# Kernel optimization log

Hardware: AMD Instinct MI355X
Metric: run time of the kernel (lower is better)

Reference implementation:

```python
import jax, jax.numpy as jnp
import numpy as np
from jax import lax

B, CIN, H, W = 8, 64, 128, 128
COUT, K = 128, 3
PAD, STRIDE, DIL = 1, 1, 1
KK = K * K


def setup_inputs() -> dict:
    ks = jax.random.split(jax.random.key(0), 6)
    x = jax.random.normal(ks[0], (B, CIN, H, W), jnp.float32)
    pre_w = jax.random.normal(ks[1], (CIN, CIN, 1, 1), jnp.float32) * (1.0 / float(np.sqrt(CIN)))
    pre_b = jnp.zeros((CIN,), jnp.float32)
    off_w = jax.random.normal(ks[2], (2 * KK, CIN, K, K), jnp.float32) * 0.01
    off_b = jnp.zeros((2 * KK,), jnp.float32)
    mod_w = jax.random.normal(ks[3], (KK, CIN, K, K), jnp.float32) * 0.01
    mod_b = jnp.zeros((KK,), jnp.float32)
    reg_w = jax.random.normal(ks[4], (COUT, CIN, K, K), jnp.float32) * (1.0 / float(np.sqrt(CIN * KK)))
    return dict(x=x, pre_w=pre_w, pre_b=pre_b, off_w=off_w, off_b=off_b,
                mod_w=mod_w, mod_b=mod_b, reg_w=reg_w)


def _conv3x3(x, w, b):
    y = lax.conv_general_dilated(x, w, (STRIDE, STRIDE), [(PAD, PAD), (PAD, PAD)],
                                 rhs_dilation=(DIL, DIL),
                                 dimension_numbers=('NCHW', 'OIHW', 'NCHW'))
    return y + b[None, :, None, None]


def _bilinear(img, py, px):
    # img: [C,H,W]; py,px: [KK,Ho,Wo] float coords; zero padding outside image
    Hh, Ww = img.shape[1], img.shape[2]
    y0f = jnp.floor(py)
    x0f = jnp.floor(px)
    wy = py - y0f
    wx = px - x0f
    y0 = y0f.astype(jnp.int32)
    x0 = x0f.astype(jnp.int32)

    def gather(yi, xi):
        valid = (yi >= 0) & (yi < Hh) & (xi >= 0) & (xi < Ww)
        yc = jnp.clip(yi, 0, Hh - 1)
        xc = jnp.clip(xi, 0, Ww - 1)
        return img[:, yc, xc] * valid[None].astype(img.dtype)  # [C,KK,Ho,Wo]

    return (gather(y0, x0) * ((1 - wy) * (1 - wx))[None]
            + gather(y0, x0 + 1) * ((1 - wy) * wx)[None]
            + gather(y0 + 1, x0) * (wy * (1 - wx))[None]
            + gather(y0 + 1, x0 + 1) * (wy * wx)[None])


def _dcn_forward(x, pre_w, pre_b, off_w, off_b, mod_w, mod_b, reg_w):
    # 1x1 channel-mapping conv created in the original forward
    x = lax.conv_general_dilated(x, pre_w, (1, 1), 'VALID',
                                 dimension_numbers=('NCHW', 'OIHW', 'NCHW'))
    x = x + pre_b[None, :, None, None]

    offset = _conv3x3(x, off_w, off_b)                    # [B,2*KK,Ho,Wo]
    mask = 2.0 * jax.nn.sigmoid(_conv3x3(x, mod_w, mod_b))  # [B,KK,Ho,Wo]

    Ho, Wo = offset.shape[2], offset.shape[3]
    off = offset.reshape(B, KK, 2, Ho, Wo)  # torchvision layout: per kernel pos (dy,dx)

    ky, kx = jnp.meshgrid(jnp.arange(K), jnp.arange(K), indexing='ij')
    base_y = (jnp.arange(Ho) * STRIDE - PAD)[None, :, None] + (ky.reshape(KK) * DIL)[:, None, None]  # [KK,Ho,1]
    base_x = (jnp.arange(Wo) * STRIDE - PAD)[None, None, :] + (kx.reshape(KK) * DIL)[:, None, None]  # [KK,1,Wo]

    py = base_y[None].astype(x.dtype) + off[:, :, 0]  # [B,KK,Ho,Wo]
    px = base_x[None].astype(x.dtype) + off[:, :, 1]

    sampled = jax.vmap(_bilinear)(x, py, px)          # [B,C,KK,Ho,Wo]
    sampled = sampled * mask[:, None]                  # modulation

    wk = reg_w.reshape(COUT, CIN, KK)
    return jnp.einsum('bckhw,ock->bohw', sampled, wk)  # [B,COUT,Ho,Wo]


def reference(x, pre_w, pre_b, off_w, off_b, mod_w, mod_b, reg_w):
    return _dcn_forward(x, pre_w, pre_b, off_w, off_b, mod_w, mod_b, reg_w)
```

## Files before the change

### kernel.cpp

```cpp
#include <hip/hip_runtime.h>
#include <hip/hip_bf16.h>
#include <cstdint>
#include <cstddef>

#define BATCH 8
#define CINC  64
#define HH    128
#define WWW   128
#define COUTC 128
#define KKC   9
#define KDIM  576
#define HWC   (HH*WWW)
#define NPX   (BATCH*HWC)

#define DT_BASE 98304

typedef float f32x4 __attribute__((ext_vector_type(4)));
typedef short bf16x8 __attribute__((ext_vector_type(8)));

static __device__ __forceinline__ unsigned short f2bf(float f){
    unsigned u = __builtin_bit_cast(unsigned, f);
    u += 0x7fffu + ((u >> 16) & 1u);
    return (unsigned short)(u >> 16);
}
static __device__ __forceinline__ float bf_lo(unsigned u){
    return __builtin_bit_cast(float, u << 16);
}
static __device__ __forceinline__ float bf_hi(unsigned u){
    return __builtin_bit_cast(float, u & 0xffff0000u);
}
static __device__ __forceinline__ unsigned cvtpk(float lo, float hi){
    unsigned r;
    asm("v_cvt_pk_bf16_f32 %0, %1, %2" : "=v"(r) : "v"(lo), "v"(hi));
    return r;
}

__global__ __launch_bounds__(256) void prep_weights(
        const float* __restrict__ off_w, const float* __restrict__ mod_w,
        const float* __restrict__ reg_w, const float* __restrict__ pre_w,
        unsigned short* __restrict__ Wb2, unsigned short* __restrict__ Wc2,
        unsigned short* __restrict__ Wp2)
{
    int idx = blockIdx.x * 256 + threadIdx.x;
    if (idx < 73728) {
        int chunk = idx >> 9, within = idx & 511;
        int lane = within >> 3, j = within & 7;
        int kk = chunk >> 4, s = (chunk >> 3) & 1, cog = chunk & 7;
        int o = cog * 16 + (lane & 15);
        int c = 32*s + 8*(lane >> 4) + j;
        Wb2[idx] = f2bf(reg_w[(o * CINC + c) * KKC + kk]);
    }
    int idx2 = idx - 73728;
    if (idx2 >= 0 && idx2 < 18432) {
        int chunk = idx2 >> 9, within = idx2 & 511;
        int lane = within >> 3, j = within & 7;
        int kk = chunk >> 2, s = (chunk >> 1) & 1, cog = chunk & 1;
        int o = cog * 16 + (lane & 15);
        int c = 32*s + 8*(lane >> 4) + j;
        float v = 0.f;
        if (o < 18)      v = off_w[(o * CINC + c) * KKC + kk];
        else if (o < 27) v = mod_w[((o - 18) * CINC + c) * KKC + kk];
        Wc2[idx2] = f2bf(v);
    }
    int idx3 = idx - 92160;
    if (idx3 >= 0 && idx3 < 4096) {
        int chunk = idx3 >> 9, within = idx3 & 511;
        int lane = within >> 3, j = within & 7;
        int s = chunk >> 2, fn = chunk & 3;
        int o = fn * 16 + (lane & 15);
        int c = 32*s + 8*(lane >> 4) + j;
        Wp2[idx3] = f2bf(pre_w[o * CINC + c]);
    }
}

__global__ __launch_bounds__(256) void conv1x1(
        const float* __restrict__ x, const unsigned short* __restrict__ Wp2,
        const float* __restrict__ pre_b, unsigned short* __restrict__ xp)
{
    __shared__ unsigned short slab[4][64 * 72];

    const int tid = threadIdx.x;
    const int lane = tid & 63;
    const int wv   = tid >> 6;
    const int l15  = lane & 15;
    const int l4   = lane >> 4;

    int bid = (int)blockIdx.x;
    int bswz = (bid & 7) * 64 + (bid >> 3);
    int pxb = bswz * 256 + wv * 64;
    int b = pxb >> 14, hw0 = pxb & 16383;
    const float* xb = x + (size_t)b * CINC * HWC + hw0;

    bf16x8 bw[4][2];
    #pragma unroll
    for (int fn = 0; fn < 4; ++fn)
        #pragma unroll
        for (int s = 0; s < 2; ++s)
            bw[fn][s] = *(const bf16x8*)(Wp2 + (size_t)(s*4 + fn) * 512 + lane * 8);
    float pb[4];
    #pragma unroll
    for (int fn = 0; fn < 4; ++fn) pb[fn] = pre_b[16*fn + l15];

    f32x4 acc[4][4];
    #pragma unroll
    for (int su = 0; su < 4; ++su)
        #pragma unroll
        for (int fn = 0; fn < 4; ++fn) acc[su][fn] = (f32x4){0.f,0.f,0.f,0.f};

    #pragma unroll
    for (int su = 0; su < 4; ++su) {
        #pragma unroll
        for (int s = 0; s < 2; ++s) {
            float f[8];
            #pragma unroll
            for (int j = 0; j < 8; ++j)
                f[j] = xb[(size_t)(s*32 + 8*l4 + j) * HWC + su*16 + l15];
            unsigned pk[4];
            #pragma unroll
            for (int d = 0; d < 4; ++d) pk[d] = cvtpk(f[2*d], f[2*d+1]);
            bf16x8 A = __builtin_bit_cast(bf16x8, make_uint4(pk[0], pk[1], pk[2], pk[3]));
            #pragma unroll
            for (int fn = 0; fn < 4; ++fn)
                acc[su][fn] = __builtin_amdgcn_mfma_f32_16x16x32_bf16(A, bw[fn][s], acc[su][fn], 0,0,0);
        }
    }

    unsigned short* sl = slab[wv];
    #pragma unroll
    for (int su = 0; su < 4; ++su)
        #pragma unroll
        for (int fn = 0; fn < 4; ++fn)
            #pragma unroll
            for (int r = 0; r < 4; ++r)
                sl[(su*16 + 4*l4 + r) * 72 + 16*fn + l15] = f2bf(acc[su][fn][r] + pb[fn]);
    const uint4* srow = (const uint4*)(sl + lane * 72);
    uint4* drow = (uint4*)(xp + (size_t)(pxb + lane) * 64);
    #pragma unroll
    for (int q = 0; q < 8; ++q) drow[q] = srow[q];
}

__global__ __launch_bounds__(512, 2) void gather_einsum(
        const unsigned short* __restrict__ xp,
        const unsigned short* __restrict__ Wb2,
        const unsigned short* __restrict__ Wc2,
        const float* __restrict__ off_b,
        const float* __restrict__ mod_b,
        float* __restrict__ out)
{
    __shared__ char smem[133120];
    char* winc = smem;
    float* epi = (float*)smem;
    float* Dt  = (float*)(smem + DT_BASE);

    const int tid  = (int)threadIdx.x;
    const int lane = tid & 63;
    const int wv   = tid >> 6;
    const int l15  = lane & 15;
    const int l4   = lane >> 4;

    int bid = (int)blockIdx.x;
    int bswz = (bid & 7) * 64 + (bid >> 3);
    const int b  = bswz >> 6;
    const int h0 = (bswz & 63) * 2;

    const unsigned short* xpb = xp + (size_t)b * HWC * CINC;

    #pragma unroll
    for (int i = 0; i < 12; ++i) {
        int c = i * 512 + tid;
        int r = c >> 10;
        int c10 = c & 1023;
        int xph = c10 >> 3, g = c10 & 7;
        int y = h0 - 2 + r;
        uint4 v = make_uint4(0u,0u,0u,0u);
        if ((unsigned)y < 128u)
            v = *(const uint4*)(xpb + ((size_t)y * 128 + xph) * 64 + g * 8);
        *(uint4*)(winc + (r*128 + xph)*128 + ((g ^ (xph & 7)) << 4)) = v;
    }
    __syncthreads();

    const int hrow = wv >> 2;
    const int x0w  = (wv & 3) * 32;
    {
        f32x4 aco[2][2];
        #pragma unroll
        for (int j = 0; j < 2; ++j)
            #pragma unroll
            for (int fn = 0; fn < 2; ++fn) aco[j][fn] = (f32x4){0.f,0.f,0.f,0.f};

        #pragma unroll
        for (int kk = 0; kk < 9; ++kk) {
            bf16x8 bc0[2], bc1[2];
            #pragma unroll
            for (int fn = 0; fn < 2; ++fn) {
                bc0[fn] = *(const bf16x8*)(Wc2 + (size_t)(kk*4     + fn) * 512 + lane * 8);
                bc1[fn] = *(const bf16x8*)(Wc2 + (size_t)(kk*4 + 2 + fn) * 512 + lane * 8);
            }
            int wr_ = hrow + (kk / 3) + 1;
            #pragma unroll
            for (int j = 0; j < 2; ++j) {
                int xx = x0w + j*16 + l15 + (kk % 3) - 1;
                bool xv = (unsigned)xx < 128u;
                int xc = xx < 0 ? 0 : (xx > 127 ? 127 : xx);
                int sx = xc & 7;
                const char* rr = winc + (wr_*128 + xc)*128;
                uint4 a0 = *(const uint4*)(rr + ((l4 ^ sx) << 4));
                uint4 a1 = *(const uint4*)(rr + (((l4+4) ^ sx) << 4));
                if (!xv) { a0 = make_uint4(0,0,0,0); a1 = make_uint4(0,0,0,0); }
                bf16x8 A0 = __builtin_bit_cast(bf16x8, a0);
                bf16x8 A1 = __builtin_bit_cast(bf16x8, a1);
                #pragma unroll
                for (int fn = 0; fn < 2; ++fn) {
                    aco[j][fn] = __builtin_amdgcn_mfma_f32_16x16x32_bf16(A0, bc0[fn], aco[j][fn], 0,0,0);
                    aco[j][fn] = __builtin_amdgcn_mfma_f32_16x16x32_bf16(A1, bc1[fn], aco[j][fn], 0,0,0);
                }
            }
        }
        #pragma unroll
        for (int j = 0; j < 2; ++j)
        #pragma unroll
        for (int fn = 0; fn < 2; ++fn) {
            int o = 16*fn + l15;
            #pragma unroll
            for (int r = 0; r < 4; ++r) {
                int pr = 4*l4 + r;
                int p  = wv*32 + j*16 + pr;
                float v = aco[j][fn][r];
                if (o < 18) {
                    v += off_b[o];
                    int k = o >> 1;
                    if ((o & 1) == 0) v += (float)(h0 + hrow - 1 + k/3);
                    else              v += (float)(x0w + j*16 + pr - 1 + (k % 3));
                } else if (o < 27) {
                    v = 2.f / (1.f + __expf(-(v + mod_b[o - 18])));
                }
                if (o < 27) Dt[p*29 + o] = v;
            }
        }
    }

    f32x4 acc[2][8];
    #pragma unroll
    for (int j = 0; j < 2; ++j)
        #pragma unroll
        for (int fn = 0; fn < 8; ++fn) acc[j][fn] = (f32x4){0.f,0.f,0.f,0.f};

    #pragma unroll 1
    for (int kk = 0; kk < 9; ++kk) {
        bf16x8 Bs0[4], Bs1[4];
        #pragma unroll
        for (int f = 0; f < 4; ++f) {
            Bs0[f] = *(const bf16x8*)(Wb2 + (size_t)(kk*16 +      f) * 512 + lane * 8);
            Bs1[f] = *(const bf16x8*)(Wb2 + (size_t)(kk*16 +  8 + f) * 512 + lane * 8);
        }

        bf16x8 A[2][2];
        #pragma unroll
        for (int j = 0; j < 2; ++j) {
            int p = wv*32 + j*16 + l15;
            float Y = Dt[p*29 + 2*kk];
            float X = Dt[p*29 + 2*kk + 1];
            float M = Dt[p*29 + 18 + kk];
            float yf = floorf(Y), xf = floorf(X);
            float wy = Y - yf, wx = X - xf;
            int y0 = (int)yf, x0i = (int)xf;
            int y1 = y0 + 1, x1 = x0i + 1;
            bool yv0 = (unsigned)y0 < 128u, yv1 = (unsigned)y1 < 128u;
            bool xv0 = (unsigned)x0i < 128u, xv1 = (unsigned)x1 < 128u;
            int xc0 = x0i < 0 ? 0 : (x0i > 127 ? 127 : x0i);
            int xc1 = x1  < 0 ? 0 : (x1  > 127 ? 127 : x1);
            int wr0 = y0 - (h0 - 2), wr1 = wr0 + 1;
            int wc0 = wr0 < 0 ? 0 : (wr0 > 5 ? 5 : wr0);
            int wc1 = wr1 < 0 ? 0 : (wr1 > 5 ? 5 : wr1);
            int s0 = xc0 & 7, s1 = xc1 & 7;

            const char* r00 = winc + (wc0*128 + xc0)*128;
            const char* r01 = winc + (wc0*128 + xc1)*128;
            const char* r10 = winc + (wc1*128 + xc0)*128;
            const char* r11 = winc + (wc1*128 + xc1)*128;
            uint4 cb0 = *(const uint4*)(r00 + ((l4 ^ s0) << 4));
            uint4 cb1 = *(const uint4*)(r00 + (((l4+4) ^ s0) << 4));
            uint4 cb2 = *(const uint4*)(r01 + ((l4 ^ s1) << 4));
            uint4 cb3 = *(const uint4*)(r01 + (((l4+4) ^ s1) << 4));
            uint4 cb4 = *(const uint4*)(r10 + ((l4 ^ s0) << 4));
            uint4 cb5 = *(const uint4*)(r10 + (((l4+4) ^ s0) << 4));
            uint4 cb6 = *(const uint4*)(r11 + ((l4 ^ s1) << 4));
            uint4 cb7 = *(const uint4*)(r11 + (((l4+4) ^ s1) << 4));

            bool oob = (yv0 && (unsigned)wr0 > 5u) || (yv1 && (unsigned)wr1 > 5u);
            if (__builtin_expect(oob, 0)) {
                int yc0 = y0 < 0 ? 0 : (y0 > 127 ? 127 : y0);
                int yc1 = y1 < 0 ? 0 : (y1 > 127 ? 127 : y1);
                const unsigned short* p00 = xpb + (size_t)(yc0*128 + xc0)*64 + 8*l4;
                const unsigned short* p01 = xpb + (size_t)(yc0*128 + xc1)*64 + 8*l4;
                const unsigned short* p10 = xpb + (size_t)(yc1*128 + xc0)*64 + 8*l4;
                const unsigned short* p11 = xpb + (size_t)(yc1*128 + xc1)*64 + 8*l4;
                cb0 = *(const uint4*)(p00);  cb1 = *(const uint4*)(p00 + 32);
                cb2 = *(const uint4*)(p01);  cb3 = *(const uint4*)(p01 + 32);
                cb4 = *(const uint4*)(p10);  cb5 = *(const uint4*)(p10 + 32);
                cb6 = *(const uint4*)(p11);  cb7 = *(const uint4*)(p11 + 32);
            }

            float u00 = (1.f - wy) * (1.f - wx) * M * ((yv0 && xv0) ? 1.f : 0.f);
            float u01 = (1.f - wy) * wx         * M * ((yv0 && xv1) ? 1.f : 0.f);
            float u10 = wy * (1.f - wx)         * M * ((yv1 && xv0) ? 1.f : 0.f);
            float u11 = wy * wx                 * M * ((yv1 && xv1) ? 1.f : 0.f);

            unsigned pk0[4], pk1[4];
            #pragma unroll
            for (int d = 0; d < 4; ++d) {
                unsigned q00, q01, q10, q11;
                q00 = cb0[d]; q01 = cb2[d]; q10 = cb4[d]; q11 = cb6[d];
                {
                    float slo = bf_lo(q00)*u00 + bf_lo(q01)*u01 + bf_lo(q10)*u10 + bf_lo(q11)*u11;
                    float shi = bf_hi(q00)*u00 + bf_hi(q01)*u01 + bf_hi(q10)*u10 + bf_hi(q11)*u11;
                    pk0[d] = cvtpk(slo, shi);
                }
                q00 = cb1[d]; q01 = cb3[d]; q10 = cb5[d]; q11 = cb7[d];
                {
                    float slo = bf_lo(q00)*u00 + bf_lo(q01)*u01 + bf_lo(q10)*u10 + bf_lo(q11)*u11;
                    float shi = bf_hi(q00)*u00 + bf_hi(q01)*u01 + bf_hi(q10)*u10 + bf_hi(q11)*u11;
                    pk1[d] = cvtpk(slo, shi);
                }
            }
            A[j][0] = __builtin_bit_cast(bf16x8, make_uint4(pk0[0], pk0[1], pk0[2], pk0[3]));
            A[j][1] = __builtin_bit_cast(bf16x8, make_uint4(pk1[0], pk1[1], pk1[2], pk1[3]));
        }

        #pragma unroll
        for (int j = 0; j < 2; ++j)
            #pragma unroll
            for (int f = 0; f < 4; ++f) {
                acc[j][f] = __builtin_amdgcn_mfma_f32_16x16x32_bf16(A[j][0], Bs0[f], acc[j][f], 0,0,0);
                acc[j][f] = __builtin_amdgcn_mfma_f32_16x16x32_bf16(A[j][1], Bs1[f], acc[j][f], 0,0,0);
            }

        #pragma unroll
        for (int f = 0; f < 4; ++f) {
            Bs0[f] = *(const bf16x8*)(Wb2 + (size_t)(kk*16 +  4 + f) * 512 + lane * 8);
            Bs1[f] = *(const bf16x8*)(Wb2 + (size_t)(kk*16 + 12 + f) * 512 + lane * 8);
        }
        #pragma unroll
        for (int j = 0; j < 2; ++j)
            #pragma unroll
            for (int f = 0; f < 4; ++f) {
                acc[j][4+f] = __builtin_amdgcn_mfma_f32_16x16x32_bf16(A[j][0], Bs0[f], acc[j][4+f], 0,0,0);
                acc[j][4+f] = __builtin_amdgcn_mfma_f32_16x16x32_bf16(A[j][1], Bs1[f], acc[j][4+f], 0,0,0);
            }
    }

    __syncthreads();
    #pragma unroll
    for (int j = 0; j < 2; ++j)
        #pragma unroll
        for (int fn = 0; fn < 8; ++fn)
            *(f32x4*)(epi + (size_t)(16*fn + l15) * 260 + 32*wv + 16*j + 4*l4) = acc[j][fn];
    __syncthreads();

    float* ob = out + (size_t)b * COUTC * HWC + h0 * 128;
    #pragma unroll
    for (int it = 0; it < 16; ++it) {
        int idx = it * 512 + tid;
        int o = idx >> 6, c = idx & 63;
        f32x4 v = *(const f32x4*)(epi + (size_t)o * 260 + 4*c);
        *(f32x4*)(ob + (size_t)o * HWC + 4*c) = v;
    }
}

extern "C" void kernel_launch(void* const* d_in, const int* in_sizes, int n_in,
                              void* d_out, int out_size, void* d_ws, size_t ws_size,
                              hipStream_t stream)
{
    const float* x     = (const float*)d_in[0];
    const float* pre_w = (const float*)d_in[1];
    const float* pre_b = (const float*)d_in[2];
    const float* off_w = (const float*)d_in[3];
    const float* off_b = (const float*)d_in[4];
    const float* mod_w = (const float*)d_in[5];
    const float* mod_b = (const float*)d_in[6];
    const float* reg_w = (const float*)d_in[7];
    float* out = (float*)d_out;

    unsigned short* xp  = (unsigned short*)d_ws;
    unsigned short* Wb2 = (unsigned short*)((char*)d_ws + 16777216);
    unsigned short* Wc2 = (unsigned short*)((char*)d_ws + 16924672);
    unsigned short* Wp2 = (unsigned short*)((char*)d_ws + 16961536);

    prep_weights<<<dim3(376), dim3(256), 0, stream>>>(off_w, mod_w, reg_w, pre_w, Wb2, Wc2, Wp2);
    conv1x1     <<<dim3(512), dim3(256), 0, stream>>>(x, Wp2, pre_b, xp);
    gather_einsum<<<dim3(512), dim3(512), 0, stream>>>(xp, Wb2, Wc2, off_b, mod_b, out);
}
```

Baseline: 83.89 us.

## Use packed f32 FMA for bilinear blend and reorder loads, unroll kk loop

The bilinear interpolation now uses v_pk_mul_f32/v_pk_fma_f32 on pairs of unpacked bf16 values, roughly halving the VALU instruction count for the blend. The LDS corner loads for both row groups are issued before the weight loads and blend, and the kk loop is unrolled by 3 so loads can overlap MFMA work. Holding cb[2][8] and the duplicated U vectors live at once raises register pressure, and building the packed operands may add v_mov instructions.

```diff
diff --git a/kernel.cpp b/kernel.cpp
--- a/kernel.cpp
+++ b/kernel.cpp
@@ -16,6 +16,7 @@
 #define DT_BASE 98304
 
 typedef float f32x4 __attribute__((ext_vector_type(4)));
+typedef float f32x2 __attribute__((ext_vector_type(2)));
 typedef short bf16x8 __attribute__((ext_vector_type(8)));
 
 static __device__ __forceinline__ unsigned short f2bf(float f){
@@ -33,6 +34,16 @@
     unsigned r;
     asm("v_cvt_pk_bf16_f32 %0, %1, %2" : "=v"(r) : "v"(lo), "v"(hi));
     return r;
+}
+static __device__ __forceinline__ f32x2 pk_mul(f32x2 a, f32x2 b){
+    f32x2 d;
+    asm("v_pk_mul_f32 %0, %1, %2" : "=v"(d) : "v"(a), "v"(b));
+    return d;
+}
+static __device__ __forceinline__ f32x2 pk_fma(f32x2 a, f32x2 b, f32x2 c){
+    f32x2 d;
+    asm("v_pk_fma_f32 %0, %1, %2, %3" : "=v"(d) : "v"(a), "v"(b), "v"(c));
+    return d;
 }
 
 __global__ __launch_bounds__(256) void prep_weights(
@@ -245,16 +256,10 @@
         #pragma unroll
         for (int fn = 0; fn < 8; ++fn) acc[j][fn] = (f32x4){0.f,0.f,0.f,0.f};
 
-    #pragma unroll 1
+    #pragma unroll 3
     for (int kk = 0; kk < 9; ++kk) {
-        bf16x8 Bs0[4], Bs1[4];
-        #pragma unroll
-        for (int f = 0; f < 4; ++f) {
-            Bs0[f] = *(const bf16x8*)(Wb2 + (size_t)(kk*16 +      f) * 512 + lane * 8);
-            Bs1[f] = *(const bf16x8*)(Wb2 + (size_t)(kk*16 +  8 + f) * 512 + lane * 8);
-        }
-
-        bf16x8 A[2][2];
+        uint4 cb[2][8];
+        f32x2 U[2][4];
         #pragma unroll
         for (int j = 0; j < 2; ++j) {
             int p = wv*32 + j*16 + l15;
@@ -278,14 +283,14 @@
             const char* r01 = winc + (wc0*128 + xc1)*128;
             const char* r10 = winc + (wc1*128 + xc0)*128;
             const char* r11 = winc + (wc1*128 + xc1)*128;
-            uint4 cb0 = *(const uint4*)(r00 + ((l4 ^ s0) << 4));
-            uint4 cb1 = *(const uint4*)(r00 + (((l4+4) ^ s0) << 4));
-            uint4 cb2 = *(const uint4*)(r01 + ((l4 ^ s1) << 4));
-            uint4 cb3 = *(const uint4*)(r01 + (((l4+4) ^ s1) << 4));
-            uint4 cb4 = *(const uint4*)(r10 + ((l4 ^ s0) << 4));
-            uint4 cb5 = *(const uint4*)(r10 + (((l4+4) ^ s0) << 4));
-            uint4 cb6 = *(const uint4*)(r11 + ((l4 ^ s1) << 4));
-            uint4 cb7 = *(const uint4*)(r11 + (((l4+4) ^ s1) << 4));
+            cb[j][0] = *(const uint4*)(r00 + ((l4 ^ s0) << 4));
+            cb[j][1] = *(const uint4*)(r00 + (((l4+4) ^ s0) << 4));
+            cb[j][2] = *(const uint4*)(r01 + ((l4 ^ s1) << 4));
+            cb[j][3] = *(const uint4*)(r01 + (((l4+4) ^ s1) << 4));
+            cb[j][4] = *(const uint4*)(r10 + ((l4 ^ s0) << 4));
+            cb[j][5] = *(const uint4*)(r10 + (((l4+4) ^ s0) << 4));
+            cb[j][6] = *(const uint4*)(r11 + ((l4 ^ s1) << 4));
+            cb[j][7] = *(const uint4*)(r11 + (((l4+4) ^ s1) << 4));
 
             bool oob = (yv0 && (unsigned)wr0 > 5u) || (yv1 && (unsigned)wr1 > 5u);
             if (__builtin_expect(oob, 0)) {
@@ -295,32 +300,60 @@
                 const unsigned short* p01 = xpb + (size_t)(yc0*128 + xc1)*64 + 8*l4;
                 const unsigned short* p10 = xpb + (size_t)(yc1*128 + xc0)*64 + 8*l4;
                 const unsigned short* p11 = xpb + (size_t)(yc1*128 + xc1)*64 + 8*l4;
-                cb0 = *(const uint4*)(p00);  cb1 = *(const uint4*)(p00 + 32);
-                cb2 = *(const uint4*)(p01);  cb3 = *(const uint4*)(p01 + 32);
-                cb4 = *(const uint4*)(p10);  cb5 = *(const uint4*)(p10 + 32);
-                cb6 = *(const uint4*)(p11);  cb7 = *(const uint4*)(p11 + 32);
+                cb[j][0] = *(const uint4*)(p00);  cb[j][1] = *(const uint4*)(p00 + 32);
+                cb[j][2] = *(const uint4*)(p01);  cb[j][3] = *(const uint4*)(p01 + 32);
+                cb[j][4] = *(const uint4*)(p10);  cb[j][5] = *(const uint4*)(p10 + 32);
+                cb[j][6] = *(const uint4*)(p11);  cb[j][7] = *(const uint4*)(p11 + 32);
             }
 
             float u00 = (1.f - wy) * (1.f - wx) * M * ((yv0 && xv0) ? 1.f : 0.f);
             float u01 = (1.f - wy) * wx         * M * ((yv0 && xv1) ? 1.f : 0.f);
             float u10 = wy * (1.f - wx)         * M * ((yv1 && xv0) ? 1.f : 0.f);
             float u11 = wy * wx                 * M * ((yv1 && xv1) ? 1.f : 0.f);
-
+            U[j][0] = (f32x2){u00, u00};
+            U[j][1] = (f32x2){u01, u01};
+            U[j][2] = (f32x2){u10, u10};
+            U[j][3] = (f32x2){u11, u11};
+        }
+
+        bf16x8 Bs0[4], Bs1[4];
+        #pragma unroll
+        for (int f = 0; f < 4; ++f) {
+            Bs0[f] = *(const bf16x8*)(Wb2 + (size_t)(kk*16 +      f) * 512 + lane * 8);
+            Bs1[f] = *(const bf16x8*)(Wb2 + (size_t)(kk*16 +  8 + f) * 512 + lane * 8);
+        }
+
+        bf16x8 A[2][2];
+        #pragma unroll
+        for (int j = 0; j < 2; ++j) {
             unsigned pk0[4], pk1[4];
             #pragma unroll
             for (int d = 0; d < 4; ++d) {
-                unsigned q00, q01, q10, q11;
-                q00 = cb0[d]; q01 = cb2[d]; q10 = cb4[d]; q11 = cb6[d];
                 {
-                    float slo = bf_lo(q00)*u00 + bf_lo(q01)*u01 + bf_lo(q10)*u10 + bf_lo(q11)*u11;
-                    float shi = bf_hi(q00)*u00 + bf_hi(q01)*u01 + bf_hi(q10)*u10 + bf_hi(q11)*u11;
-                    pk0[d] = cvtpk(slo, shi);
+                    unsigned q00 = cb[j][0][d], q01 = cb[j][2][d];
+                    unsigned q10 = cb[j][4][d], q11 = cb[j][6][d];
+                    f32x2 P00 = (f32x2){bf_lo(q00), bf_hi(q00)};
+                    f32x2 P01 = (f32x2){bf_lo(q01), bf_hi(q01)};
+                    f32x2 P10 = (f32x2){bf_lo(q10), bf_hi(q10)};
+                    f32x2 P11 = (f32x2){bf_lo(q11), bf_hi(q11)};
+                    f32x2 S = pk_fma(P11, U[j][3],
+                              pk_fma(P10, U[j][2],
+                              pk_fma(P01, U[j][1],
+                              pk_mul(P00, U[j][0]))));
+                    pk0[d] = cvtpk(S.x, S.y);
                 }
-                q00 = cb1[d]; q01 = cb3[d]; q10 = cb5[d]; q11 = cb7[d];
                 {
-                    float slo = bf_lo(q00)*u00 + bf_lo(q01)*u01 + bf_lo(q10)*u10 + bf_lo(q11)*u11;
-                    float shi = bf_hi(q00)*u00 + bf_hi(q01)*u01 + bf_hi(q10)*u10 + bf_hi(q11)*u11;
-                    pk1[d] = cvtpk(slo, shi);
+                    unsigned q00 = cb[j][1][d], q01 = cb[j][3][d];
+                    unsigned q10 = cb[j][5][d], q11 = cb[j][7][d];
+                    f32x2 P00 = (f32x2){bf_lo(q00), bf_hi(q00)};
+                    f32x2 P01 = (f32x2){bf_lo(q01), bf_hi(q01)};
+                    f32x2 P10 = (f32x2){bf_lo(q10), bf_hi(q10)};
+                    f32x2 P11 = (f32x2){bf_lo(q11), bf_hi(q11)};
+                    f32x2 S = pk_fma(P11, U[j][3],
+                              pk_fma(P10, U[j][2],
+                              pk_fma(P01, U[j][1],
+                              pk_mul(P00, U[j][0]))));
+                    pk1[d] = cvtpk(S.x, S.y);
                 }
             }
             A[j][0] = __builtin_bit_cast(bf16x8, make_uint4(pk0[0], pk0[1], pk0[2], pk0[3]));
@@ -334,7 +367,6 @@
                 acc[j][f] = __builtin_amdgcn_mfma_f32_16x16x32_bf16(A[j][0], Bs0[f], acc[j][f], 0,0,0);
                 acc[j][f] = __builtin_amdgcn_mfma_f32_16x16x32_bf16(A[j][1], Bs1[f], acc[j][f], 0,0,0);
             }
-
         #pragma unroll
         for (int f = 0; f < 4; ++f) {
             Bs0[f] = *(const bf16x8*)(Wb2 + (size_t)(kk*16 +  4 + f) * 512 + lane * 8);
```

Result: no change. 84.49 us (+0.7%).

## Halve gather tile width, keep offsets in registers via lane shuffles

Applied to the files above, without the earlier changes.

The fused gather+einsum kernel now runs 1024 blocks of 256 threads, each covering 2 rows by 64 columns. This shrinks the LDS window to 48KB so three blocks fit per CU. The offset/mask conv swaps its MFMA operands so results land per pixel-column, then redistributes them with xor-shuffle butterflies into registers, removing the Dt LDS table. Samples outside the narrower window fall back to global loads, and the epilogue stages output in two halves through a smaller LDS buffer. The risks are more boundary fallbacks, more halo reloads, higher register pressure from the unrolled kk loop, and extra barriers.

```diff
diff --git a/kernel.cpp b/kernel.cpp
--- a/kernel.cpp
+++ b/kernel.cpp
@@ -13,7 +13,8 @@
 #define HWC   (HH*WWW)
 #define NPX   (BATCH*HWC)
 
-#define DT_BASE 98304
+#define WIN_W 64
+#define LDS_SZ (6*WIN_W*128)
 
 typedef float f32x4 __attribute__((ext_vector_type(4)));
 typedef short bf16x8 __attribute__((ext_vector_type(8)));
@@ -35,10 +36,12 @@
     return r;
 }
 
+#define IDX(o) (16*((((o)&15)>>2)>>1) + 8*((((o)&15)>>2)&1) + 4*((o)>>4) + ((o)&3))
+
 __global__ __launch_bounds__(256) void prep_weights(
         const float* __restrict__ off_w, const float* __restrict__ mod_w,
         const float* __restrict__ reg_w, const float* __restrict__ pre_w,
-        unsigned short* __restrict__ Wb2, unsigned short* __restrict__ Wc2,
+        unsigned short* __restrict__ Wb2, unsigned short* __restrict__ Wc3,
         unsigned short* __restrict__ Wp2)
 {
     int idx = blockIdx.x * 256 + threadIdx.x;
@@ -54,13 +57,13 @@
     if (idx2 >= 0 && idx2 < 18432) {
         int chunk = idx2 >> 9, within = idx2 & 511;
         int lane = within >> 3, j = within & 7;
-        int kk = chunk >> 2, s = (chunk >> 1) & 1, cog = chunk & 1;
-        int o = cog * 16 + (lane & 15);
+        int kk = chunk >> 2, s = (chunk >> 1) & 1, t = chunk & 1;
+        int o = 16*t + (lane & 15);
         int c = 32*s + 8*(lane >> 4) + j;
         float v = 0.f;
         if (o < 18)      v = off_w[(o * CINC + c) * KKC + kk];
         else if (o < 27) v = mod_w[((o - 18) * CINC + c) * KKC + kk];
-        Wc2[idx2] = f2bf(v);
+        Wc3[idx2] = f2bf(v);
     }
     int idx3 = idx - 92160;
     if (idx3 >= 0 && idx3 < 4096) {
@@ -139,18 +142,17 @@
     for (int q = 0; q < 8; ++q) drow[q] = srow[q];
 }
 
-__global__ __launch_bounds__(512, 2) void gather_einsum(
+__global__ __launch_bounds__(256, 3) void gather_einsum(
         const unsigned short* __restrict__ xp,
         const unsigned short* __restrict__ Wb2,
-        const unsigned short* __restrict__ Wc2,
+        const unsigned short* __restrict__ Wc3,
         const float* __restrict__ off_b,
         const float* __restrict__ mod_b,
         float* __restrict__ out)
 {
-    __shared__ char smem[133120];
+    __shared__ char smem[LDS_SZ];
     char* winc = smem;
     float* epi = (float*)smem;
-    float* Dt  = (float*)(smem + DT_BASE);
 
     const int tid  = (int)threadIdx.x;
     const int lane = tid & 63;
@@ -159,84 +161,127 @@
     const int l4   = lane >> 4;
 
     int bid = (int)blockIdx.x;
-    int bswz = (bid & 7) * 64 + (bid >> 3);
-    const int b  = bswz >> 6;
-    const int h0 = (bswz & 63) * 2;
+    int bswz = (bid & 7) * 128 + (bid >> 3);
+    const int b   = bswz >> 7;
+    const int rem = bswz & 127;
+    const int h0  = (rem >> 1) << 1;
+    const int x0w = (rem & 1) << 6;
 
     const unsigned short* xpb = xp + (size_t)b * HWC * CINC;
 
     #pragma unroll
     for (int i = 0; i < 12; ++i) {
-        int c = i * 512 + tid;
-        int r = c >> 10;
-        int c10 = c & 1023;
-        int xph = c10 >> 3, g = c10 & 7;
+        int c = i * 256 + tid;
+        int r = c >> 9;
+        int cr = c & 511;
+        int wx = cr >> 3, g = cr & 7;
         int y = h0 - 2 + r;
         uint4 v = make_uint4(0u,0u,0u,0u);
         if ((unsigned)y < 128u)
-            v = *(const uint4*)(xpb + ((size_t)y * 128 + xph) * 64 + g * 8);
-        *(uint4*)(winc + (r*128 + xph)*128 + ((g ^ (xph & 7)) << 4)) = v;
+            v = *(const uint4*)(xpb + ((size_t)y * 128 + x0w + wx) * 64 + g * 8);
+        *(uint4*)(winc + (r*WIN_W + wx)*128 + ((g ^ (wx & 7)) << 4)) = v;
     }
     __syncthreads();
 
-    const int hrow = wv >> 2;
-    const int x0w  = (wv & 3) * 32;
+    const int hrow = wv >> 1;
+    const int xsl  = (wv & 1) * 32;
+    float cy[2][9], cx[2][9], cm[2][9];
     {
         f32x4 aco[2][2];
         #pragma unroll
         for (int j = 0; j < 2; ++j)
             #pragma unroll
-            for (int fn = 0; fn < 2; ++fn) aco[j][fn] = (f32x4){0.f,0.f,0.f,0.f};
+            for (int t = 0; t < 2; ++t) aco[j][t] = (f32x4){0.f,0.f,0.f,0.f};
 
         #pragma unroll
         for (int kk = 0; kk < 9; ++kk) {
-            bf16x8 bc0[2], bc1[2];
-            #pragma unroll
-            for (int fn = 0; fn < 2; ++fn) {
-                bc0[fn] = *(const bf16x8*)(Wc2 + (size_t)(kk*4     + fn) * 512 + lane * 8);
-                bc1[fn] = *(const bf16x8*)(Wc2 + (size_t)(kk*4 + 2 + fn) * 512 + lane * 8);
-            }
-            int wr_ = hrow + (kk / 3) + 1;
+            bf16x8 wa[2][2];
+            #pragma unroll
+            for (int s = 0; s < 2; ++s)
+                #pragma unroll
+                for (int t = 0; t < 2; ++t)
+                    wa[s][t] = *(const bf16x8*)(Wc3 + (size_t)(kk*4 + s*2 + t) * 512 + lane * 8);
+            int dx = kk % 3 - 1;
+            int y_ = h0 + hrow + kk/3 - 1;
+            bool yv = (unsigned)y_ < 128u;
+            int wr_ = hrow + kk/3 + 1;
             #pragma unroll
             for (int j = 0; j < 2; ++j) {
-                int xx = x0w + j*16 + l15 + (kk % 3) - 1;
-                bool xv = (unsigned)xx < 128u;
-                int xc = xx < 0 ? 0 : (xx > 127 ? 127 : xx);
-                int sx = xc & 7;
-                const char* rr = winc + (wr_*128 + xc)*128;
-                uint4 a0 = *(const uint4*)(rr + ((l4 ^ sx) << 4));
-                uint4 a1 = *(const uint4*)(rr + (((l4+4) ^ sx) << 4));
-                if (!xv) { a0 = make_uint4(0,0,0,0); a1 = make_uint4(0,0,0,0); }
-                bf16x8 A0 = __builtin_bit_cast(bf16x8, a0);
-                bf16x8 A1 = __builtin_bit_cast(bf16x8, a1);
+                int gx  = x0w + xsl + 16*j + l15;
+                int gxx = gx + dx;
+                int wx = gxx - x0w;
+                bool in_win = (unsigned)wx < (unsigned)WIN_W;
+                int wxc = wx < 0 ? 0 : (wx > WIN_W-1 ? WIN_W-1 : wx);
+                int sx = wxc & 7;
+                const char* rr = winc + (wr_*WIN_W + wxc)*128;
+                uint4 b0 = *(const uint4*)(rr + ((l4 ^ sx) << 4));
+                uint4 b1 = *(const uint4*)(rr + (((l4+4) ^ sx) << 4));
+                if (__builtin_expect(!in_win, 0)) {
+                    bool v = yv && ((unsigned)gxx < 128u);
+                    const unsigned short* gp = xpb
+                        + (size_t)(((y_ & 127) * 128) + (gxx & 127)) * 64 + 8*l4;
+                    uint4 z = make_uint4(0u,0u,0u,0u);
+                    b0 = v ? *(const uint4*)(gp)      : z;
+                    b1 = v ? *(const uint4*)(gp + 32) : z;
+                }
+                bf16x8 B0 = __builtin_bit_cast(bf16x8, b0);
+                bf16x8 B1 = __builtin_bit_cast(bf16x8, b1);
                 #pragma unroll
-                for (int fn = 0; fn < 2; ++fn) {
-                    aco[j][fn] = __builtin_amdgcn_mfma_f32_16x16x32_bf16(A0, bc0[fn], aco[j][fn], 0,0,0);
-                    aco[j][fn] = __builtin_amdgcn_mfma_f32_16x16x32_bf16(A1, bc1[fn], aco[j][fn], 0,0,0);
+                for (int t = 0; t < 2; ++t) {
+                    aco[j][t] = __builtin_amdgcn_mfma_f32_16x16x32_bf16(wa[0][t], B0, aco[j][t], 0,0,0);
+                    aco[j][t] = __builtin_amdgcn_mfma_f32_16x16x32_bf16(wa[1][t], B1, aco[j][t], 0,0,0);
                 }
             }
         }
-        #pragma unroll
-        for (int j = 0; j < 2; ++j)
-        #pragma unroll
-        for (int fn = 0; fn < 2; ++fn) {
-            int o = 16*fn + l15;
-            #pragma unroll
-            for (int r = 0; r < 4; ++r) {
-                int pr = 4*l4 + r;
-                int p  = wv*32 + j*16 + pr;
-                float v = aco[j][fn][r];
+
+        float e0[8], e1[8];
+        #pragma unroll
+        for (int t = 0; t < 2; ++t)
+        #pragma unroll
+        for (int r = 0; r < 4; ++r) {
+            int o = 16*t + 4*l4 + r;
+            #pragma unroll
+            for (int j = 0; j < 2; ++j) {
+                float v = aco[j][t][r];
+                int gx = x0w + xsl + 16*j + l15;
                 if (o < 18) {
                     v += off_b[o];
                     int k = o >> 1;
                     if ((o & 1) == 0) v += (float)(h0 + hrow - 1 + k/3);
-                    else              v += (float)(x0w + j*16 + pr - 1 + (k % 3));
+                    else              v += (float)(gx - 1 + (k - (k/3)*3));
                 } else if (o < 27) {
                     v = 2.f / (1.f + __expf(-(v + mod_b[o - 18])));
                 }
-                if (o < 27) Dt[p*29 + o] = v;
-            }
-        }
+                if (j == 0) e0[4*t + r] = v; else e1[4*t + r] = v;
+            }
+        }
+
+        const bool hb0 = (l4 & 1) != 0;
+        const bool hb1 = (l4 & 2) != 0;
+        #define BFLY(eA, jj) do {                                             \
+            float f_[16], g_[32];                                             \
+            _Pragma("unroll")                                                 \
+            for (int i = 0; i < 8; ++i) {                                     \
+                float p = __shfl_xor(eA[i], 16);                              \
+                f_[i]   = hb0 ? p : eA[i];                                    \
+                f_[8+i] = hb0 ? eA[i] : p;                                    \
+            }                                                                 \
+            _Pragma("unroll")                                                 \
+            for (int i = 0; i < 16; ++i) {                                    \
+                float p = __shfl_xor(f_[i], 32);                              \
+                g_[i]    = hb1 ? p : f_[i];                                   \
+                g_[16+i] = hb1 ? f_[i] : p;                                   \
+            }                                                                 \
+            _Pragma("unroll")                                                 \
+            for (int k = 0; k < 9; ++k) {                                     \
+                cy[jj][k] = g_[IDX(2*k)];                                     \
+                cx[jj][k] = g_[IDX(2*k + 1)];                                 \
+                cm[jj][k] = g_[IDX(18 + k)];                                  \
+            }                                                                 \
+        } while (0)
+        BFLY(e0, 0);
+        BFLY(e1, 1);
+        #undef BFLY
     }
 
     f32x4 acc[2][8];
@@ -245,7 +290,7 @@
         #pragma unroll
         for (int fn = 0; fn < 8; ++fn) acc[j][fn] = (f32x4){0.f,0.f,0.f,0.f};
 
-    #pragma unroll 1
+    #pragma unroll
     for (int kk = 0; kk < 9; ++kk) {
         bf16x8 Bs0[4], Bs1[4];
         #pragma unroll
@@ -257,27 +302,27 @@
         bf16x8 A[2][2];
         #pragma unroll
         for (int j = 0; j < 2; ++j) {
-            int p = wv*32 + j*16 + l15;
-            float Y = Dt[p*29 + 2*kk];
-            float X = Dt[p*29 + 2*kk + 1];
-            float M = Dt[p*29 + 18 + kk];
+            float Y = cy[j][kk], X = cx[j][kk], M = cm[j][kk];
             float yf = floorf(Y), xf = floorf(X);
             float wy = Y - yf, wx = X - xf;
             int y0 = (int)yf, x0i = (int)xf;
             int y1 = y0 + 1, x1 = x0i + 1;
             bool yv0 = (unsigned)y0 < 128u, yv1 = (unsigned)y1 < 128u;
             bool xv0 = (unsigned)x0i < 128u, xv1 = (unsigned)x1 < 128u;
-            int xc0 = x0i < 0 ? 0 : (x0i > 127 ? 127 : x0i);
-            int xc1 = x1  < 0 ? 0 : (x1  > 127 ? 127 : x1);
             int wr0 = y0 - (h0 - 2), wr1 = wr0 + 1;
+            int wxi = x0i - x0w;
+            bool inW0 = (unsigned)wxi < (unsigned)WIN_W;
+            bool inW1 = (unsigned)(wxi + 1) < (unsigned)WIN_W;
             int wc0 = wr0 < 0 ? 0 : (wr0 > 5 ? 5 : wr0);
             int wc1 = wr1 < 0 ? 0 : (wr1 > 5 ? 5 : wr1);
-            int s0 = xc0 & 7, s1 = xc1 & 7;
-
-            const char* r00 = winc + (wc0*128 + xc0)*128;
-            const char* r01 = winc + (wc0*128 + xc1)*128;
-            const char* r10 = winc + (wc1*128 + xc0)*128;
-            const char* r11 = winc + (wc1*128 + xc1)*128;
+            int wx0 = wxi < 0 ? 0 : (wxi > WIN_W-1 ? WIN_W-1 : wxi);
+            int wx1 = wxi+1 < 0 ? 0 : (wxi+1 > WIN_W-1 ? WIN_W-1 : wxi+1);
+            int s0 = wx0 & 7, s1 = wx1 & 7;
+
+            const char* r00 = winc + (wc0*WIN_W + wx0)*128;
+            const char* r01 = winc + (wc0*WIN_W + wx1)*128;
+            const char* r10 = winc + (wc1*WIN_W + wx0)*128;
+            const char* r11 = winc + (wc1*WIN_W + wx1)*128;
             uint4 cb0 = *(const uint4*)(r00 + ((l4 ^ s0) << 4));
             uint4 cb1 = *(const uint4*)(r00 + (((l4+4) ^ s0) << 4));
             uint4 cb2 = *(const uint4*)(r01 + ((l4 ^ s1) << 4));
@@ -287,10 +332,13 @@
             uint4 cb6 = *(const uint4*)(r11 + ((l4 ^ s1) << 4));
             uint4 cb7 = *(const uint4*)(r11 + (((l4+4) ^ s1) << 4));
 
-            bool oob = (yv0 && (unsigned)wr0 > 5u) || (yv1 && (unsigned)wr1 > 5u);
+            bool oob = (yv0 && (unsigned)wr0 > 5u) || (yv1 && (unsigned)wr1 > 5u)
+                    || (xv0 && !inW0) || (xv1 && !inW1);
             if (__builtin_expect(oob, 0)) {
                 int yc0 = y0 < 0 ? 0 : (y0 > 127 ? 127 : y0);
                 int yc1 = y1 < 0 ? 0 : (y1 > 127 ? 127 : y1);
+                int xc0 = x0i < 0 ? 0 : (x0i > 127 ? 127 : x0i);
+                int xc1 = x1  < 0 ? 0 : (x1  > 127 ? 127 : x1);
                 const unsigned short* p00 = xpb + (size_t)(yc0*128 + xc0)*64 + 8*l4;
                 const unsigned short* p01 = xpb + (size_t)(yc0*128 + xc1)*64 + 8*l4;
                 const unsigned short* p10 = xpb + (size_t)(yc1*128 + xc0)*64 + 8*l4;
@@ -334,7 +382,6 @@
                 acc[j][f] = __builtin_amdgcn_mfma_f32_16x16x32_bf16(A[j][0], Bs0[f], acc[j][f], 0,0,0);
                 acc[j][f] = __builtin_amdgcn_mfma_f32_16x16x32_bf16(A[j][1], Bs1[f], acc[j][f], 0,0,0);
             }
-
         #pragma unroll
         for (int f = 0; f < 4; ++f) {
             Bs0[f] = *(const bf16x8*)(Wb2 + (size_t)(kk*16 +  4 + f) * 512 + lane * 8);
@@ -351,19 +398,25 @@
 
     __syncthreads();
     #pragma unroll
-    for (int j = 0; j < 2; ++j)
-        #pragma unroll
-        for (int fn = 0; fn < 8; ++fn)
-            *(f32x4*)(epi + (size_t)(16*fn + l15) * 260 + 32*wv + 16*j + 4*l4) = acc[j][fn];
-    __syncthreads();
-
-    float* ob = out + (size_t)b * COUTC * HWC + h0 * 128;
-    #pragma unroll
-    for (int it = 0; it < 16; ++it) {
-        int idx = it * 512 + tid;
-        int o = idx >> 6, c = idx & 63;
-        f32x4 v = *(const f32x4*)(epi + (size_t)o * 260 + 4*c);
-        *(f32x4*)(ob + (size_t)o * HWC + 4*c) = v;
+    for (int half = 0; half < 2; ++half) {
+        #pragma unroll
+        for (int j = 0; j < 2; ++j)
+            #pragma unroll
+            for (int ff = 0; ff < 4; ++ff)
+                *(f32x4*)(epi + (size_t)(16*ff + l15) * 130 + 32*wv + 16*j + 4*l4)
+                    = acc[j][4*half + ff];
+        __syncthreads();
+        float* ob = out + (size_t)b * COUTC * HWC + (size_t)(64*half) * HWC
+                  + h0 * 128 + x0w;
+        #pragma unroll
+        for (int it = 0; it < 8; ++it) {
+            int idx = it * 256 + tid;
+            int col = idx >> 5, q = idx & 31;
+            int p = 4 * q;
+            f32x4 v = *(const f32x4*)(epi + (size_t)col * 130 + p);
+            *(f32x4*)(ob + (size_t)col * HWC + (p >> 6) * 128 + (p & 63)) = v;
+        }
+        __syncthreads();
     }
 }
 
@@ -383,10 +436,10 @@
 
     unsigned short* xp  = (unsigned short*)d_ws;
     unsigned short* Wb2 = (unsigned short*)((char*)d_ws + 16777216);
-    unsigned short* Wc2 = (unsigned short*)((char*)d_ws + 16924672);
+    unsigned short* Wc3 = (unsigned short*)((char*)d_ws + 16924672);
     unsigned short* Wp2 = (unsigned short*)((char*)d_ws + 16961536);
 
-    prep_weights<<<dim3(376), dim3(256), 0, stream>>>(off_w, mod_w, reg_w, pre_w, Wb2, Wc2, Wp2);
+    prep_weights<<<dim3(376), dim3(256), 0, stream>>>(off_w, mod_w, reg_w, pre_w, Wb2, Wc3, Wp2);
     conv1x1     <<<dim3(512), dim3(256), 0, stream>>>(x, Wp2, pre_b, xp);
-    gather_einsum<<<dim3(512), dim3(512), 0, stream>>>(xp, Wb2, Wc2, off_b, mod_b, out);
-}
+    gather_einsum<<<dim3(1024), dim3(256), 0, stream>>>(xp, Wb2, Wc3, off_b, mod_b, out);
+}
```

Measured after the change: 116.4 us. +38.7%, slower.
